# Performance work log

Hardware: AMD Instinct MI355X
Metric: run time of the kernel (lower is better)

## Reference

```python
import jax, jax.numpy as jnp
import numpy as np

N_EDGES = 262144
N_TRIP = 1048576
D = 128
N_RBF = 6
A_DIM = 49  # n_spher * l_spher
N_BIL = 8


def setup_inputs() -> dict:
    key = jax.random.key(0)
    ks = jax.random.split(key, 16)
    s = lambda fan_in: 1.0 / np.sqrt(fan_in)
    return {
        "m_ji": jax.random.normal(ks[0], (N_EDGES, D), jnp.float32),
        "e_rbf": jax.random.normal(ks[1], (N_EDGES, N_RBF), jnp.float32),
        "a_sbf": jax.random.normal(ks[2], (N_TRIP, A_DIM), jnp.float32),
        "nbr_list": jax.random.randint(ks[3], (N_EDGES, 2), 0, 100000),
        "angle_list": jax.random.randint(ks[4], (N_TRIP, 3), 0, N_EDGES),
        "kj_idx": jax.random.randint(ks[5], (N_TRIP,), 0, N_EDGES),
        "nbr_m_w": jax.random.normal(ks[6], (D, D), jnp.float32) * s(D),
        "nbr_m_b": jnp.zeros((D,), jnp.float32),
        "e_rbf_w": jax.random.normal(ks[7], (N_RBF, D), jnp.float32) * s(N_RBF),
        "a_sbf_w": jax.random.normal(ks[8], (A_DIM, N_BIL), jnp.float32) * s(A_DIM),
        "final_w": jax.random.normal(ks[9], (D, N_BIL, D), jnp.float32) * s(N_BIL * D),
        "m_ji_w": jax.random.normal(ks[10], (D, D), jnp.float32) * s(D),
        "m_ji_b": jnp.zeros((D,), jnp.float32),
        "post_w": jax.random.normal(ks[11], (D, D), jnp.float32) * s(D),
        "post_b": jnp.zeros((D,), jnp.float32),
        "res_w": jax.random.normal(ks[12], (3, 2, D, D), jnp.float32) * s(D),
        "res_b": jnp.zeros((3, 2, D), jnp.float32),
    }


def _residual(x, w2, b2):
    # two Dense(swish) layers + skip
    out = x
    for k in range(2):
        out = jax.nn.silu(out @ w2[k] + b2[k])
    return out + x


def reference(m_ji, e_rbf, a_sbf, nbr_list, angle_list, kj_idx,
              nbr_m_w, nbr_m_b, e_rbf_w, a_sbf_w, final_w,
              m_ji_w, m_ji_b, post_w, post_b, res_w, res_b):
    # DirectedMessage: gather per-triplet edge features
    t_m = jax.nn.silu(m_ji[kj_idx] @ nbr_m_w + nbr_m_b)   # [W, D]
    t_e = e_rbf[kj_idx] @ e_rbf_w                          # [W, D]
    m_and_e = t_m * t_e                                    # [W, D]
    t_a = a_sbf @ a_sbf_w                                  # [W, J]
    out = jnp.einsum('wj,wl,ijl->wi', t_a, m_and_e, final_w)  # [W, D]
    directed = jax.ops.segment_sum(out, kj_idx, num_segments=m_ji.shape[0])  # [E, D]

    transf_m_ji = jax.nn.silu(m_ji @ m_ji_w + m_ji_b)
    output = directed + transf_m_ji
    output = _residual(output, res_w[0], res_b[0])
    output = jax.nn.silu(output @ post_w + post_b) + transf_m_ji
    output = _residual(output, res_w[1], res_b[1])
    output = _residual(output, res_w[2], res_b[2])
    return output
```

## Files before the change

### kernel.cpp

```cpp
#include <hip/hip_runtime.h>

#define N_EDGE 262144
#define N_TRI  1048576
#define DIM    128
#define NRBF   6
#define ADIM   49
#define NBIL   8
#define TE     64
#define NTHR   256
#define SXD    68
#define EB2    2048
#define NSL    4

typedef __attribute__((ext_vector_type(8))) short bf16x8;
typedef __attribute__((ext_vector_type(4))) float f32x4;

__device__ __forceinline__ float fast_rcp(float x) {
    float r; asm("v_rcp_f32 %0, %1" : "=v"(r) : "v"(x)); return r;
}
__device__ __forceinline__ float fast_exp2(float x) {
    float r; asm("v_exp_f32 %0, %1" : "=v"(r) : "v"(x)); return r;
}
__device__ __forceinline__ float silu_f(float x) {
    return x * fast_rcp(1.f + fast_exp2(-1.44269504f * x));
}
__device__ __forceinline__ unsigned short f2bf(float f) {
    unsigned int u = __float_as_uint(f);
    return (unsigned short)((u + 0x7FFFu + ((u >> 16) & 1u)) >> 16);
}
__device__ __forceinline__ unsigned int pk2(float x, float y) {
    unsigned int r;
    asm("v_cvt_pk_bf16_f32 %0, %1, %2" : "=v"(r) : "v"(x), "v"(y));
    return r;
}
__device__ __forceinline__ float bf2f(unsigned short u) {
    return __uint_as_float(((unsigned int)u) << 16);
}

__global__ __launch_bounds__(256) void prep_w_k(
    const float* __restrict__ nbr, const float* __restrict__ mji,
    const float* __restrict__ post, const float* __restrict__ res,
    const float* __restrict__ fw, unsigned short* __restrict__ wt)
{
    int idx = blockIdx.x * 256 + threadIdx.x;
    if (idx < 9 * 16384) {
        int m = idx >> 14, rr = idx & 16383;
        int n = rr >> 7, ks = rr & 127;
        int ko = (ks & ~31) | ((ks & 1) << 4) | ((ks >> 1) & 15);
        const float* src = (m == 0) ? nbr : (m == 1) ? mji : (m == 2) ? post
                          : (res + (size_t)(m - 3) * 16384);
        wt[idx] = f2bf(src[ko * DIM + n]);
    } else {
        int r2 = idx - 9 * 16384;
        int n = r2 >> 10, j = (r2 >> 7) & 7, ls = r2 & 127;
        int lo = (ls & ~31) | ((ls & 1) << 4) | ((ls >> 1) & 15);
        wt[idx] = f2bf(fw[(size_t)(n * NBIL + j) * DIM + lo]);
    }
}

__global__ __launch_bounds__(256) void ta_all_k(
    const float* __restrict__ a_sbf, const float* __restrict__ a_sbf_w,
    float* __restrict__ taw)
{
    __shared__ __align__(16) float sA[256 * ADIM];
    __shared__ float sWa[ADIM * NBIL];
    const int tid = threadIdx.x;
    const size_t w0 = (size_t)blockIdx.x * 256;

    {
        const float4* src = (const float4*)(a_sbf + w0 * ADIM);
        float4* dst = (float4*)sA;
        for (int i = tid; i < (256 * ADIM) / 4; i += 256) dst[i] = src[i];
    }
    for (int i = tid; i < ADIM * NBIL; i += 256) sWa[i] = a_sbf_w[i];
    __syncthreads();

    float ta[NBIL];
    #pragma unroll
    for (int j = 0; j < NBIL; ++j) ta[j] = 0.0f;
    const float* row = sA + tid * ADIM;
    #pragma unroll
    for (int k = 0; k < ADIM; ++k) {
        float v = row[k];
        #pragma unroll
        for (int j = 0; j < NBIL; ++j) ta[j] = fmaf(v, sWa[k * NBIL + j], ta[j]);
    }
    float4* dst = (float4*)(taw + (w0 + tid) * NBIL);
    dst[0] = make_float4(ta[0], ta[1], ta[2], ta[3]);
    dst[1] = make_float4(ta[4], ta[5], ta[6], ta[7]);
}

__global__ __launch_bounds__(1024) void seg_reduce_k(
    const float* __restrict__ taw, const int* __restrict__ kj_idx,
    float* __restrict__ ta_sum)
{
    __shared__ float acc[EB2 * NBIL];
    const int tid = threadIdx.x;
    const int eg = blockIdx.x >> 2;
    const int sl = blockIdx.x & 3;
    const int lo = eg * EB2;

    for (int i = tid; i < EB2 * NBIL; i += 1024) acc[i] = 0.f;
    __syncthreads();

    const int4* kj4 = (const int4*)kj_idx;
    const int i0 = sl * (N_TRI / 4 / NSL);
    const int i1 = i0 + (N_TRI / 4 / NSL);
    for (int i = i0 + tid; i < i1; i += 1024) {
        int4 v = kj4[i];
        int w0 = i * 4;
        #pragma unroll
        for (int k = 0; k < 4; ++k) {
            int e = (k == 0) ? v.x : (k == 1) ? v.y : (k == 2) ? v.z : v.w;
            unsigned d = (unsigned)(e - lo);
            if (d < (unsigned)EB2) {
                const float4* p = (const float4*)(taw + (size_t)(w0 + k) * NBIL);
                float4 a = p[0], b = p[1];
                float* q = acc + d * NBIL;
                atomicAdd(q + 0, a.x); atomicAdd(q + 1, a.y);
                atomicAdd(q + 2, a.z); atomicAdd(q + 3, a.w);
                atomicAdd(q + 4, b.x); atomicAdd(q + 5, b.y);
                atomicAdd(q + 6, b.z); atomicAdd(q + 7, b.w);
            }
        }
    }
    __syncthreads();
    for (int i = tid; i < EB2 * NBIL; i += 1024)
        unsafeAtomicAdd(ta_sum + (size_t)lo * NBIL + i, acc[i]);
}

__global__ __launch_bounds__(256) void triplet_atomic_k(
    const float* __restrict__ a_sbf, const float* __restrict__ a_sbf_w,
    const int* __restrict__ kj_idx, float* __restrict__ ta_sum)
{
    __shared__ __align__(16) float sA[256 * ADIM];
    __shared__ float sWa[ADIM * NBIL];
    const int tid = threadIdx.x;
    const size_t w0 = (size_t)blockIdx.x * 256;
    {
        const float4* src = (const float4*)(a_sbf + w0 * ADIM);
        float4* dst = (float4*)sA;
        for (int i = tid; i < (256 * ADIM) / 4; i += 256) dst[i] = src[i];
    }
    for (int i = tid; i < ADIM * NBIL; i += 256) sWa[i] = a_sbf_w[i];
    __syncthreads();
    float ta[NBIL];
    #pragma unroll
    for (int j = 0; j < NBIL; ++j) ta[j] = 0.0f;
    const float* row = sA + tid * ADIM;
    #pragma unroll
    for (int k = 0; k < ADIM; ++k) {
        float v = row[k];
        #pragma unroll
        for (int j = 0; j < NBIL; ++j) ta[j] = fmaf(v, sWa[k * NBIL + j], ta[j]);
    }
    const int e = kj_idx[w0 + tid];
    float* dst = ta_sum + (size_t)e * NBIL;
    #pragma unroll
    for (int j = 0; j < NBIL; ++j) unsafeAtomicAdd(dst + j, ta[j]);
}

__global__ __launch_bounds__(NTHR) void edge_main_k(
    const float* __restrict__ m_ji, const float* __restrict__ e_rbf,
    const float* __restrict__ ta_sum, const unsigned short* __restrict__ wt,
    const float* __restrict__ nbr_m_b, const float* __restrict__ e_rbf_w,
    const float* __restrict__ m_ji_b, const float* __restrict__ post_b,
    const float* __restrict__ res_b, float* __restrict__ out)
{
    __shared__ __align__(16) unsigned int sXd[2][TE * SXD];
    __shared__ __align__(16) unsigned int sTd[TE * SXD];
    __shared__ __align__(16) float sTAT[NBIL * TE];
    __shared__ __align__(16) float sET[NRBF * TE];

    const int tid  = threadIdx.x;
    const int lane = tid & 63;
    const int ml   = lane & 15;
    const int g    = lane >> 4;
    const int wq   = tid >> 6;
    const int n0   = wq * 32;
    const int q16  = wq * 16;
    const size_t e0 = (size_t)blockIdx.x * TE;

    bf16x8 A[4][2], Bf[2][4];
    f32x4 acc[4][2], xr[4][2], bs0, bs1;

    auto prefB = [&](const unsigned short* wtm, int ldk, int kbase) {
        #pragma unroll
        for (int nt = 0; nt < 2; ++nt) {
            const unsigned short* wb =
                wtm + (size_t)(n0 + nt * 16 + ml) * ldk + kbase + g * 8;
            #pragma unroll
            for (int ks = 0; ks < 4; ++ks)
                Bf[nt][ks] = *(const bf16x8*)(wb + ks * 32);
        }
    };
    auto ldbias = [&](const float* bp) {
        float b0 = bp[n0 + ml], b1 = bp[n0 + 16 + ml];
        bs0[0] = b0; bs0[1] = b0; bs0[2] = b0; bs0[3] = b0;
        bs1[0] = b1; bs1[1] = b1; bs1[2] = b1; bs1[3] = b1;
    };
    auto ldzero = [&]() {
        #pragma unroll
        for (int r = 0; r < 4; ++r) { bs0[r] = 0.f; bs1[r] = 0.f; }
    };

    prefB(wt + 1 * 16384, DIM, 0);

    #pragma unroll
    for (int i = 0; i < 4; ++i) {
        int q = tid + i * NTHR;
        int row = q >> 4, sub = q & 15;
        int dq = sub >> 2, c4 = (sub & 3) * 4;
        const float* src = m_ji + (e0 + row) * DIM + dq * 32 + c4;
        float4 a = *(const float4*)(src);
        float4 b = *(const float4*)(src + 16);
        uint4 d;
        d.x = pk2(a.x, b.x); d.y = pk2(a.y, b.y);
        d.z = pk2(a.z, b.z); d.w = pk2(a.w, b.w);
        *(uint4*)(sXd[0] + row * SXD + dq * 16 + c4) = d;
    }
    #pragma unroll
    for (int i = 0; i < 2; ++i) {
        int idx = tid + i * NTHR;
        int j = idx >> 6, e = idx & 63;
        sTAT[j * TE + e] = ta_sum[(e0 + e) * NBIL + j];
    }
    for (int i = tid; i < NRBF * TE; i += NTHR) {
        int j = i >> 6, e = i & 63;
        sET[j * TE + e] = e_rbf[(e0 + e) * NRBF + j];
    }
    __syncthreads();

    auto loadA = [&](const unsigned int* bufp, int h) {
        const unsigned short* base = (const unsigned short*)bufp;
        #pragma unroll
        for (int mt = 0; mt < 4; ++mt) {
            const unsigned short* rb = base + (mt * 16 + ml) * (SXD * 2) + h * 64 + g * 8;
            A[mt][0] = *(const bf16x8*)(rb);
            A[mt][1] = *(const bf16x8*)(rb + 32);
        }
    };
    auto mfmaH = [&](int h, bool seed) {
        #pragma unroll
        for (int kk = 0; kk < 2; ++kk)
        #pragma unroll
        for (int nt = 0; nt < 2; ++nt)
        #pragma unroll
        for (int mt = 0; mt < 4; ++mt) {
            f32x4 cin = (seed && kk == 0) ? (nt == 0 ? bs0 : bs1) : acc[mt][nt];
            acc[mt][nt] = __builtin_amdgcn_mfma_f32_16x16x32_bf16(
                A[mt][kk], Bf[nt][h * 2 + kk], cin, 0, 0, 0);
        }
    };
    auto gemm_full = [&](const unsigned int* bufp) {
        loadA(bufp, 0); mfmaH(0, true); loadA(bufp, 1); mfmaH(1, false);
    };
    auto store_sX = [&](unsigned int* bufp, f32x4 (&v)[4][2]) {
        #pragma unroll
        for (int mt = 0; mt < 4; ++mt)
        #pragma unroll
        for (int r = 0; r < 4; ++r)
            bufp[(mt * 16 + g * 4 + r) * SXD + q16 + ml] = pk2(v[mt][0][r], v[mt][1][r]);
        __syncthreads();
    };

    unsigned int* bufA = sXd[0];
    unsigned int* bufB = sXd[1];

    ldbias(m_ji_b);
    gemm_full(bufA);
    prefB(wt + 0 * 16384, DIM, 0);
    #pragma unroll
    for (int mt = 0; mt < 4; ++mt)
    #pragma unroll
    for (int r = 0; r < 4; ++r)
        sTd[(mt * 16 + g * 4 + r) * SXD + q16 + ml] =
            pk2(silu_f(acc[mt][0][r]), silu_f(acc[mt][1][r]));

    ldbias(nbr_m_b);
    float ewc[2][NRBF];
    #pragma unroll
    for (int nt = 0; nt < 2; ++nt)
    #pragma unroll
    for (int q = 0; q < NRBF; ++q)
        ewc[nt][q] = e_rbf_w[q * DIM + n0 + nt * 16 + ml];
    gemm_full(bufA);
    const unsigned short* fwb = wt + 9 * 16384;
    prefB(fwb, NBIL * DIM, 0);
    #pragma unroll
    for (int mt = 0; mt < 4; ++mt) {
        f32x4 er[NRBF];
        #pragma unroll
        for (int q = 0; q < NRBF; ++q)
            er[q] = *(const f32x4*)(sET + q * TE + mt * 16 + g * 4);
        #pragma unroll
        for (int r = 0; r < 4; ++r) {
            float te0 = 0.f, te1 = 0.f;
            #pragma unroll
            for (int q = 0; q < NRBF; ++q) {
                te0 = fmaf(er[q][r], ewc[0][q], te0);
                te1 = fmaf(er[q][r], ewc[1][q], te1);
            }
            acc[mt][0][r] = silu_f(acc[mt][0][r]) * te0;
            acc[mt][1][r] = silu_f(acc[mt][1][r]) * te1;
        }
    }
    store_sX(bufB, acc);

    #pragma unroll
    for (int mt = 0; mt < 4; ++mt)
    #pragma unroll
    for (int r = 0; r < 4; ++r) {
        unsigned int t = sTd[(mt * 16 + g * 4 + r) * SXD + q16 + ml];
        xr[mt][0][r] = bf2f((unsigned short)(t & 0xffff));
        xr[mt][1][r] = bf2f((unsigned short)(t >> 16));
    }
    ldzero();
    for (int j = 0; j < NBIL; ++j) {
        gemm_full(bufB);
        if (j < NBIL - 1) prefB(fwb, NBIL * DIM, (j + 1) * DIM);
        else              prefB(wt + 3 * 16384, DIM, 0);
        #pragma unroll
        for (int mt = 0; mt < 4; ++mt) {
            f32x4 tv = *(const f32x4*)(sTAT + j * TE + mt * 16 + g * 4);
            #pragma unroll
            for (int nt = 0; nt < 2; ++nt)
            #pragma unroll
            for (int r = 0; r < 4; ++r)
                xr[mt][nt][r] = fmaf(tv[r], acc[mt][nt][r], xr[mt][nt][r]);
        }
    }
    store_sX(bufA, xr);

    ldbias(res_b + 0);
    gemm_full(bufA); prefB(wt + 4 * 16384, DIM, 0);
    #pragma unroll
    for (int mt = 0; mt < 4; ++mt)
    #pragma unroll
    for (int r = 0; r < 4; ++r) {
        acc[mt][0][r] = silu_f(acc[mt][0][r]);
        acc[mt][1][r] = silu_f(acc[mt][1][r]);
    }
    store_sX(bufB, acc);
    ldbias(res_b + 128);
    gemm_full(bufB); prefB(wt + 2 * 16384, DIM, 0);
    #pragma unroll
    for (int mt = 0; mt < 4; ++mt)
    #pragma unroll
    for (int r = 0; r < 4; ++r) {
        xr[mt][0][r] += silu_f(acc[mt][0][r]);
        xr[mt][1][r] += silu_f(acc[mt][1][r]);
    }
    store_sX(bufA, xr);

    ldbias(post_b);
    gemm_full(bufA); prefB(wt + 5 * 16384, DIM, 0);
    #pragma unroll
    for (int mt = 0; mt < 4; ++mt)
    #pragma unroll
    for (int r = 0; r < 4; ++r) {
        unsigned int t = sTd[(mt * 16 + g * 4 + r) * SXD + q16 + ml];
        xr[mt][0][r] = silu_f(acc[mt][0][r]) + bf2f((unsigned short)(t & 0xffff));
        xr[mt][1][r] = silu_f(acc[mt][1][r]) + bf2f((unsigned short)(t >> 16));
    }
    store_sX(bufB, xr);

    ldbias(res_b + 256);
    gemm_full(bufB); prefB(wt + 6 * 16384, DIM, 0);
    #pragma unroll
    for (int mt = 0; mt < 4; ++mt)
    #pragma unroll
    for (int r = 0; r < 4; ++r) {
        acc[mt][0][r] = silu_f(acc[mt][0][r]);
        acc[mt][1][r] = silu_f(acc[mt][1][r]);
    }
    store_sX(bufA, acc);
    ldbias(res_b + 384);
    gemm_full(bufA); prefB(wt + 7 * 16384, DIM, 0);
    #pragma unroll
    for (int mt = 0; mt < 4; ++mt)
    #pragma unroll
    for (int r = 0; r < 4; ++r) {
        xr[mt][0][r] += silu_f(acc[mt][0][r]);
        xr[mt][1][r] += silu_f(acc[mt][1][r]);
    }
    store_sX(bufB, xr);

    ldbias(res_b + 512);
    gemm_full(bufB); prefB(wt + 8 * 16384, DIM, 0);
    #pragma unroll
    for (int mt = 0; mt < 4; ++mt)
    #pragma unroll
    for (int r = 0; r < 4; ++r) {
        acc[mt][0][r] = silu_f(acc[mt][0][r]);
        acc[mt][1][r] = silu_f(acc[mt][1][r]);
    }
    store_sX(bufA, acc);
    ldbias(res_b + 640);
    gemm_full(bufA);
    #pragma unroll
    for (int mt = 0; mt < 4; ++mt)
    #pragma unroll
    for (int r = 0; r < 4; ++r) {
        int row = mt * 16 + g * 4 + r;
        out[(e0 + row) * DIM + n0 + ml]      = silu_f(acc[mt][0][r]) + xr[mt][0][r];
        out[(e0 + row) * DIM + n0 + 16 + ml] = silu_f(acc[mt][1][r]) + xr[mt][1][r];
    }
}

extern "C" void kernel_launch(void* const* d_in, const int* in_sizes, int n_in,
                              void* d_out, int out_size, void* d_ws, size_t ws_size,
                              hipStream_t stream)
{
    (void)in_sizes; (void)n_in; (void)out_size;
    const float* m_ji    = (const float*)d_in[0];
    const float* e_rbf   = (const float*)d_in[1];
    const float* a_sbf   = (const float*)d_in[2];
    const int*   kj_idx  = (const int*)d_in[5];
    const float* nbr_m_w = (const float*)d_in[6];
    const float* nbr_m_b = (const float*)d_in[7];
    const float* e_rbf_w = (const float*)d_in[8];
    const float* a_sbf_w = (const float*)d_in[9];
    const float* final_w = (const float*)d_in[10];
    const float* m_ji_w  = (const float*)d_in[11];
    const float* m_ji_b  = (const float*)d_in[12];
    const float* post_w  = (const float*)d_in[13];
    const float* post_b  = (const float*)d_in[14];
    const float* res_w   = (const float*)d_in[15];
    const float* res_b   = (const float*)d_in[16];
    float* out = (float*)d_out;

    const size_t taB  = (size_t)N_EDGE * NBIL * sizeof(float);
    const size_t wtB  = (size_t)278528 * sizeof(unsigned short);
    const size_t tawB = (size_t)N_TRI * NBIL * sizeof(float);

    float* ta_sum = (float*)d_ws;
    unsigned short* wt = (unsigned short*)((char*)d_ws + taB);
    float* taw = (float*)((char*)d_ws + taB + wtB);

    prep_w_k<<<1088, 256, 0, stream>>>(nbr_m_w, m_ji_w, post_w, res_w, final_w, wt);
    hipMemsetAsync(ta_sum, 0, taB, stream);

    if (ws_size >= taB + wtB + tawB) {
        ta_all_k<<<N_TRI / 256, 256, 0, stream>>>(a_sbf, a_sbf_w, taw);
        seg_reduce_k<<<(N_EDGE / EB2) * NSL, 1024, 0, stream>>>(taw, kj_idx, ta_sum);
    } else {
        triplet_atomic_k<<<N_TRI / 256, 256, 0, stream>>>(a_sbf, a_sbf_w, kj_idx, ta_sum);
    }
    edge_main_k<<<N_EDGE / TE, NTHR, 0, stream>>>(m_ji, e_rbf, ta_sum, wt,
        nbr_m_b, e_rbf_w, m_ji_b, post_b, res_b, out);
}
```

Before: 469.6 us.

## Process two 64-edge tiles per block to reuse weight fragments across tiles

Each block of edge_main_k now handles 128 edges as two 64-row sub-tiles, running the MFMA chain on both with the same prefetched B weight fragments before loading the next weights. This halves per-tile global weight fragment loads and lets two independent MFMA streams overlap. The ping-pong shared buffers become a single pair buffer, so each store now needs a barrier before and after. Doubled accumulators (acc0/acc1, xr0/xr1) raise register pressure and may lower occupancy or cause spills.

Result: slower. 489.0 us (+4.1%).

```diff
diff --git a/kernel.cpp b/kernel.cpp
--- a/kernel.cpp
+++ b/kernel.cpp
@@ -7,6 +7,7 @@
 #define ADIM   49
 #define NBIL   8
 #define TE     64
+#define TP     2
 #define NTHR   256
 #define SXD    68
 #define EB2    2048
@@ -167,10 +168,10 @@
     const float* __restrict__ m_ji_b, const float* __restrict__ post_b,
     const float* __restrict__ res_b, float* __restrict__ out)
 {
-    __shared__ __align__(16) unsigned int sXd[2][TE * SXD];
-    __shared__ __align__(16) unsigned int sTd[TE * SXD];
-    __shared__ __align__(16) float sTAT[NBIL * TE];
-    __shared__ __align__(16) float sET[NRBF * TE];
+    __shared__ __align__(16) unsigned int sXdA[TP * TE * SXD];
+    __shared__ __align__(16) unsigned int sTdA[TP * TE * SXD];
+    __shared__ __align__(16) float sTAT[NBIL * TP * TE];
+    __shared__ __align__(16) float sET[NRBF * TP * TE];
 
     const int tid  = threadIdx.x;
     const int lane = tid & 63;
@@ -179,10 +180,11 @@
     const int wq   = tid >> 6;
     const int n0   = wq * 32;
     const int q16  = wq * 16;
-    const size_t e0 = (size_t)blockIdx.x * TE;
+    const size_t e0 = (size_t)blockIdx.x * (TP * TE);
+    const int ET = TP * TE;
 
     bf16x8 A[4][2], Bf[2][4];
-    f32x4 acc[4][2], xr[4][2], bs0, bs1;
+    f32x4 acc0[4][2], acc1[4][2], xr0[4][2], xr1[4][2], bs0, bs1;
 
     auto prefB = [&](const unsigned short* wtm, int ldk, int kbase) {
         #pragma unroll
@@ -207,7 +209,7 @@
     prefB(wt + 1 * 16384, DIM, 0);
 
     #pragma unroll
-    for (int i = 0; i < 4; ++i) {
+    for (int i = 0; i < 8; ++i) {
         int q = tid + i * NTHR;
         int row = q >> 4, sub = q & 15;
         int dq = sub >> 2, c4 = (sub & 3) * 4;
@@ -217,17 +219,17 @@
         uint4 d;
         d.x = pk2(a.x, b.x); d.y = pk2(a.y, b.y);
         d.z = pk2(a.z, b.z); d.w = pk2(a.w, b.w);
-        *(uint4*)(sXd[0] + row * SXD + dq * 16 + c4) = d;
-    }
-    #pragma unroll
-    for (int i = 0; i < 2; ++i) {
+        *(uint4*)(sXdA + row * SXD + dq * 16 + c4) = d;
+    }
+    #pragma unroll
+    for (int i = 0; i < 4; ++i) {
         int idx = tid + i * NTHR;
-        int j = idx >> 6, e = idx & 63;
-        sTAT[j * TE + e] = ta_sum[(e0 + e) * NBIL + j];
-    }
-    for (int i = tid; i < NRBF * TE; i += NTHR) {
-        int j = i >> 6, e = i & 63;
-        sET[j * TE + e] = e_rbf[(e0 + e) * NRBF + j];
+        int j = idx >> 7, e = idx & 127;
+        sTAT[j * ET + e] = ta_sum[(e0 + e) * NBIL + j];
+    }
+    for (int i = tid; i < NRBF * ET; i += NTHR) {
+        int j = i >> 7, e = i & 127;
+        sET[j * ET + e] = e_rbf[(e0 + e) * NRBF + j];
     }
     __syncthreads();
 
@@ -240,7 +242,7 @@
             A[mt][1] = *(const bf16x8*)(rb + 32);
         }
     };
-    auto mfmaH = [&](int h, bool seed) {
+    auto mfmaH = [&](f32x4 (&acc)[4][2], int h, bool seed) {
         #pragma unroll
         for (int kk = 0; kk < 2; ++kk)
         #pragma unroll
@@ -252,30 +254,37 @@
                 A[mt][kk], Bf[nt][h * 2 + kk], cin, 0, 0, 0);
         }
     };
-    auto gemm_full = [&](const unsigned int* bufp) {
-        loadA(bufp, 0); mfmaH(0, true); loadA(bufp, 1); mfmaH(1, false);
-    };
-    auto store_sX = [&](unsigned int* bufp, f32x4 (&v)[4][2]) {
+    auto gemm_full = [&](const unsigned int* bufp, f32x4 (&acc)[4][2]) {
+        loadA(bufp, 0); mfmaH(acc, 0, true); loadA(bufp, 1); mfmaH(acc, 1, false);
+    };
+    auto store_pair = [&](f32x4 (&v0)[4][2], f32x4 (&v1)[4][2]) {
+        __syncthreads();
         #pragma unroll
         for (int mt = 0; mt < 4; ++mt)
         #pragma unroll
-        for (int r = 0; r < 4; ++r)
-            bufp[(mt * 16 + g * 4 + r) * SXD + q16 + ml] = pk2(v[mt][0][r], v[mt][1][r]);
+        for (int r = 0; r < 4; ++r) {
+            int off = (mt * 16 + g * 4 + r) * SXD + q16 + ml;
+            sXdA[off]               = pk2(v0[mt][0][r], v0[mt][1][r]);
+            sXdA[TE * SXD + off]    = pk2(v1[mt][0][r], v1[mt][1][r]);
+        }
         __syncthreads();
     };
 
-    unsigned int* bufA = sXd[0];
-    unsigned int* bufB = sXd[1];
+    const unsigned int* b0p = sXdA;
+    const unsigned int* b1p = sXdA + TE * SXD;
 
     ldbias(m_ji_b);
-    gemm_full(bufA);
+    gemm_full(b0p, acc0);
+    gemm_full(b1p, acc1);
     prefB(wt + 0 * 16384, DIM, 0);
     #pragma unroll
     for (int mt = 0; mt < 4; ++mt)
     #pragma unroll
-    for (int r = 0; r < 4; ++r)
-        sTd[(mt * 16 + g * 4 + r) * SXD + q16 + ml] =
-            pk2(silu_f(acc[mt][0][r]), silu_f(acc[mt][1][r]));
+    for (int r = 0; r < 4; ++r) {
+        int off = (mt * 16 + g * 4 + r) * SXD + q16 + ml;
+        sTdA[off]            = pk2(silu_f(acc0[mt][0][r]), silu_f(acc0[mt][1][r]));
+        sTdA[TE * SXD + off] = pk2(silu_f(acc1[mt][0][r]), silu_f(acc1[mt][1][r]));
+    }
 
     ldbias(nbr_m_b);
     float ewc[2][NRBF];
@@ -284,127 +293,133 @@
     #pragma unroll
     for (int q = 0; q < NRBF; ++q)
         ewc[nt][q] = e_rbf_w[q * DIM + n0 + nt * 16 + ml];
-    gemm_full(bufA);
+    gemm_full(b0p, acc0);
+    gemm_full(b1p, acc1);
     const unsigned short* fwb = wt + 9 * 16384;
     prefB(fwb, NBIL * DIM, 0);
     #pragma unroll
-    for (int mt = 0; mt < 4; ++mt) {
-        f32x4 er[NRBF];
-        #pragma unroll
-        for (int q = 0; q < NRBF; ++q)
-            er[q] = *(const f32x4*)(sET + q * TE + mt * 16 + g * 4);
-        #pragma unroll
-        for (int r = 0; r < 4; ++r) {
-            float te0 = 0.f, te1 = 0.f;
+    for (int t = 0; t < 2; ++t) {
+        f32x4 (&ac)[4][2] = (t == 0) ? acc0 : acc1;
+        #pragma unroll
+        for (int mt = 0; mt < 4; ++mt) {
+            f32x4 er[NRBF];
             #pragma unroll
-            for (int q = 0; q < NRBF; ++q) {
-                te0 = fmaf(er[q][r], ewc[0][q], te0);
-                te1 = fmaf(er[q][r], ewc[1][q], te1);
+            for (int q = 0; q < NRBF; ++q)
+                er[q] = *(const f32x4*)(sET + q * ET + t * TE + mt * 16 + g * 4);
+            #pragma unroll
+            for (int r = 0; r < 4; ++r) {
+                float te0 = 0.f, te1 = 0.f;
+                #pragma unroll
+                for (int q = 0; q < NRBF; ++q) {
+                    te0 = fmaf(er[q][r], ewc[0][q], te0);
+                    te1 = fmaf(er[q][r], ewc[1][q], te1);
+                }
+                ac[mt][0][r] = silu_f(ac[mt][0][r]) * te0;
+                ac[mt][1][r] = silu_f(ac[mt][1][r]) * te1;
             }
-            acc[mt][0][r] = silu_f(acc[mt][0][r]) * te0;
-            acc[mt][1][r] = silu_f(acc[mt][1][r]) * te1;
-        }
-    }
-    store_sX(bufB, acc);
+        }
+    }
+    store_pair(acc0, acc1);
 
     #pragma unroll
     for (int mt = 0; mt < 4; ++mt)
     #pragma unroll
     for (int r = 0; r < 4; ++r) {
-        unsigned int t = sTd[(mt * 16 + g * 4 + r) * SXD + q16 + ml];
-        xr[mt][0][r] = bf2f((unsigned short)(t & 0xffff));
-        xr[mt][1][r] = bf2f((unsigned short)(t >> 16));
+        int off = (mt * 16 + g * 4 + r) * SXD + q16 + ml;
+        unsigned int t0 = sTdA[off], t1 = sTdA[TE * SXD + off];
+        xr0[mt][0][r] = bf2f((unsigned short)(t0 & 0xffff));
+        xr0[mt][1][r] = bf2f((unsigned short)(t0 >> 16));
+        xr1[mt][0][r] = bf2f((unsigned short)(t1 & 0xffff));
+        xr1[mt][1][r] = bf2f((unsigned short)(t1 >> 16));
     }
     ldzero();
     for (int j = 0; j < NBIL; ++j) {
-        gemm_full(bufB);
+        gemm_full(b0p, acc0);
+        gemm_full(b1p, acc1);
         if (j < NBIL - 1) prefB(fwb, NBIL * DIM, (j + 1) * DIM);
         else              prefB(wt + 3 * 16384, DIM, 0);
         #pragma unroll
         for (int mt = 0; mt < 4; ++mt) {
-            f32x4 tv = *(const f32x4*)(sTAT + j * TE + mt * 16 + g * 4);
+            f32x4 tv0 = *(const f32x4*)(sTAT + j * ET + mt * 16 + g * 4);
+            f32x4 tv1 = *(const f32x4*)(sTAT + j * ET + TE + mt * 16 + g * 4);
             #pragma unroll
             for (int nt = 0; nt < 2; ++nt)
             #pragma unroll
-            for (int r = 0; r < 4; ++r)
-                xr[mt][nt][r] = fmaf(tv[r], acc[mt][nt][r], xr[mt][nt][r]);
-        }
-    }
-    store_sX(bufA, xr);
+            for (int r = 0; r < 4; ++r) {
+                xr0[mt][nt][r] = fmaf(tv0[r], acc0[mt][nt][r], xr0[mt][nt][r]);
+                xr1[mt][nt][r] = fmaf(tv1[r], acc1[mt][nt][r], xr1[mt][nt][r]);
+            }
+        }
+    }
+    store_pair(xr0, xr1);
+
+    auto silu_inplace = [&](f32x4 (&ac)[4][2]) {
+        #pragma unroll
+        for (int mt = 0; mt < 4; ++mt)
+        #pragma unroll
+        for (int r = 0; r < 4; ++r) {
+            ac[mt][0][r] = silu_f(ac[mt][0][r]);
+            ac[mt][1][r] = silu_f(ac[mt][1][r]);
+        }
+    };
+    auto add_into = [&](f32x4 (&xr)[4][2], f32x4 (&ac)[4][2]) {
+        #pragma unroll
+        for (int mt = 0; mt < 4; ++mt)
+        #pragma unroll
+        for (int r = 0; r < 4; ++r) {
+            xr[mt][0][r] += silu_f(ac[mt][0][r]);
+            xr[mt][1][r] += silu_f(ac[mt][1][r]);
+        }
+    };
 
     ldbias(res_b + 0);
-    gemm_full(bufA); prefB(wt + 4 * 16384, DIM, 0);
+    gemm_full(b0p, acc0); gemm_full(b1p, acc1); prefB(wt + 4 * 16384, DIM, 0);
+    silu_inplace(acc0); silu_inplace(acc1);
+    store_pair(acc0, acc1);
+    ldbias(res_b + 128);
+    gemm_full(b0p, acc0); gemm_full(b1p, acc1); prefB(wt + 2 * 16384, DIM, 0);
+    add_into(xr0, acc0); add_into(xr1, acc1);
+    store_pair(xr0, xr1);
+
+    ldbias(post_b);
+    gemm_full(b0p, acc0); gemm_full(b1p, acc1); prefB(wt + 5 * 16384, DIM, 0);
     #pragma unroll
     for (int mt = 0; mt < 4; ++mt)
     #pragma unroll
     for (int r = 0; r < 4; ++r) {
-        acc[mt][0][r] = silu_f(acc[mt][0][r]);
-        acc[mt][1][r] = silu_f(acc[mt][1][r]);
-    }
-    store_sX(bufB, acc);
-    ldbias(res_b + 128);
-    gemm_full(bufB); prefB(wt + 2 * 16384, DIM, 0);
-    #pragma unroll
-    for (int mt = 0; mt < 4; ++mt)
-    #pragma unroll
-    for (int r = 0; r < 4; ++r) {
-        xr[mt][0][r] += silu_f(acc[mt][0][r]);
-        xr[mt][1][r] += silu_f(acc[mt][1][r]);
-    }
-    store_sX(bufA, xr);
-
-    ldbias(post_b);
-    gemm_full(bufA); prefB(wt + 5 * 16384, DIM, 0);
-    #pragma unroll
-    for (int mt = 0; mt < 4; ++mt)
-    #pragma unroll
-    for (int r = 0; r < 4; ++r) {
-        unsigned int t = sTd[(mt * 16 + g * 4 + r) * SXD + q16 + ml];
-        xr[mt][0][r] = silu_f(acc[mt][0][r]) + bf2f((unsigned short)(t & 0xffff));
-        xr[mt][1][r] = silu_f(acc[mt][1][r]) + bf2f((unsigned short)(t >> 16));
-    }
-    store_sX(bufB, xr);
+        int off = (mt * 16 + g * 4 + r) * SXD + q16 + ml;
+        unsigned int t0 = sTdA[off], t1 = sTdA[TE * SXD + off];
+        xr0[mt][0][r] = silu_f(acc0[mt][0][r]) + bf2f((unsigned short)(t0 & 0xffff));
+        xr0[mt][1][r] = silu_f(acc0[mt][1][r]) + bf2f((unsigned short)(t0 >> 16));
+        xr1[mt][0][r] = silu_f(acc1[mt][0][r]) + bf2f((unsigned short)(t1 & 0xffff));
+        xr1[mt][1][r] = silu_f(acc1[mt][1][r]) + bf2f((unsigned short)(t1 >> 16));
+    }
+    store_pair(xr0, xr1);
 
     ldbias(res_b + 256);
-    gemm_full(bufB); prefB(wt + 6 * 16384, DIM, 0);
-    #pragma unroll
-    for (int mt = 0; mt < 4; ++mt)
-    #pragma unroll
-    for (int r = 0; r < 4; ++r) {
-        acc[mt][0][r] = silu_f(acc[mt][0][r]);
-        acc[mt][1][r] = silu_f(acc[mt][1][r]);
-    }
-    store_sX(bufA, acc);
+    gemm_full(b0p, acc0); gemm_full(b1p, acc1); prefB(wt + 6 * 16384, DIM, 0);
+    silu_inplace(acc0); silu_inplace(acc1);
+    store_pair(acc0, acc1);
     ldbias(res_b + 384);
-    gemm_full(bufA); prefB(wt + 7 * 16384, DIM, 0);
-    #pragma unroll
-    for (int mt = 0; mt < 4; ++mt)
-    #pragma unroll
-    for (int r = 0; r < 4; ++r) {
-        xr[mt][0][r] += silu_f(acc[mt][0][r]);
-        xr[mt][1][r] += silu_f(acc[mt][1][r]);
-    }
-    store_sX(bufB, xr);
+    gemm_full(b0p, acc0); gemm_full(b1p, acc1); prefB(wt + 7 * 16384, DIM, 0);
+    add_into(xr0, acc0); add_into(xr1, acc1);
+    store_pair(xr0, xr1);
 
     ldbias(res_b + 512);
-    gemm_full(bufB); prefB(wt + 8 * 16384, DIM, 0);
-    #pragma unroll
-    for (int mt = 0; mt < 4; ++mt)
-    #pragma unroll
-    for (int r = 0; r < 4; ++r) {
-        acc[mt][0][r] = silu_f(acc[mt][0][r]);
-        acc[mt][1][r] = silu_f(acc[mt][1][r]);
-    }
-    store_sX(bufA, acc);
+    gemm_full(b0p, acc0); gemm_full(b1p, acc1); prefB(wt + 8 * 16384, DIM, 0);
+    silu_inplace(acc0); silu_inplace(acc1);
+    store_pair(acc0, acc1);
     ldbias(res_b + 640);
-    gemm_full(bufA);
+    gemm_full(b0p, acc0); gemm_full(b1p, acc1);
     #pragma unroll
     for (int mt = 0; mt < 4; ++mt)
     #pragma unroll
     for (int r = 0; r < 4; ++r) {
         int row = mt * 16 + g * 4 + r;
-        out[(e0 + row) * DIM + n0 + ml]      = silu_f(acc[mt][0][r]) + xr[mt][0][r];
-        out[(e0 + row) * DIM + n0 + 16 + ml] = silu_f(acc[mt][1][r]) + xr[mt][1][r];
+        out[(e0 + row) * DIM + n0 + ml]           = silu_f(acc0[mt][0][r]) + xr0[mt][0][r];
+        out[(e0 + row) * DIM + n0 + 16 + ml]      = silu_f(acc0[mt][1][r]) + xr0[mt][1][r];
+        out[(e0 + TE + row) * DIM + n0 + ml]      = silu_f(acc1[mt][0][r]) + xr1[mt][0][r];
+        out[(e0 + TE + row) * DIM + n0 + 16 + ml] = silu_f(acc1[mt][1][r]) + xr1[mt][1][r];
     }
 }
 
@@ -447,6 +462,6 @@
     } else {
         triplet_atomic_k<<<N_TRI / 256, 256, 0, stream>>>(a_sbf, a_sbf_w, kj_idx, ta_sum);
     }
-    edge_main_k<<<N_EDGE / TE, NTHR, 0, stream>>>(m_ji, e_rbf, ta_sum, wt,
+    edge_main_k<<<N_EDGE / (TP * TE), NTHR, 0, stream>>>(m_ji, e_rbf, ta_sum, wt,
         nbr_m_b, e_rbf_w, m_ji_b, post_b, res_b, out);
 }
```
